# Kernel tuning notes

Measured on AMD Instinct MI355X. Metric: run time of the kernel, lower is better.

## Reference

```python
import jax, jax.numpy as jnp
import numpy as np

N = 100000   # nodes
E = 1600000  # edges (avg degree 16)
IN = 128     # in_channels
H = 64       # num_hidden -> conv1 out = 2*H = 128
RRELU_SLOPE = (1.0 / 8.0 + 1.0 / 3.0) / 2.0  # F.rrelu eval: mean of (lower, upper)


def setup_inputs() -> dict:
    key = jax.random.key(0)
    k1, k2, k3, k4 = jax.random.split(key, 4)
    x = jax.random.normal(k1, (N, IN), dtype=jnp.float32)
    edge_index = jax.random.randint(k2, (2, E), 0, N, dtype=jnp.int32)
    # Glorot-ish init for the two GCN linear layers (PyG GCNConv has weight + bias)
    W1 = jax.random.normal(k3, (IN, 2 * H), dtype=jnp.float32) * (1.0 / np.sqrt(IN))
    b1 = jnp.zeros((2 * H,), dtype=jnp.float32)
    W2 = jax.random.normal(k4, (2 * H, H), dtype=jnp.float32) * (1.0 / np.sqrt(2 * H))
    b2 = jnp.zeros((H,), dtype=jnp.float32)
    return {"x": x, "edge_index": edge_index, "W1": W1, "b1": b1, "W2": W2, "b2": b2}


def _gcn_conv(x, row, col, norm, W, b, n):
    # PyG GCNConv: transform, gather source nodes, scale by sym norm, scatter-add to targets
    h = x @ W                                   # [N, out]
    msg = h[row] * norm[:, None]                # [E+N, out] gathered messages
    return jax.ops.segment_sum(msg, col, num_segments=n) + b


def reference(x, edge_index, W1, b1, W2, b2):
    n = x.shape[0]
    loops = jnp.arange(n, dtype=edge_index.dtype)
    row = jnp.concatenate([edge_index[0], loops])  # sources (with self-loops)
    col = jnp.concatenate([edge_index[1], loops])  # targets (with self-loops)
    deg = jax.ops.segment_sum(jnp.ones_like(col, dtype=x.dtype), col, num_segments=n)
    dinv = jnp.where(deg > 0, jax.lax.rsqrt(deg), 0.0)
    norm = dinv[row] * dinv[col]                  # deg^{-1/2}[u] * deg^{-1/2}[v]
    h = _gcn_conv(x, row, col, norm, W1, b1, n)
    h = jnp.where(h >= 0, h, RRELU_SLOPE * h)     # rrelu (eval mode)
    return _gcn_conv(h, row, col, norm, W2, b2, n)
```

## Files before the change

### kernel.cpp

```cpp
#include <hip/hip_runtime.h>


#define C_IN   128
#define C_MID  128
#define C_OUT2 64
#define SLOT_CAP 64
#define SORT_SH  9
#define SORT_W   196
#define SORT_CAP 16384
#define P1_EPT   8

typedef __attribute__((ext_vector_type(8))) short short8;
typedef __attribute__((ext_vector_type(4))) float floatx4;
typedef __attribute__((ext_vector_type(2))) float f32x2;

__device__ __constant__ float kSlope = 0.22916666666666666f;

__device__ __forceinline__ unsigned short f2bf(float f) {
    unsigned u = __builtin_bit_cast(unsigned, f);
    u = (u + 0x7fffu + ((u >> 16) & 1u)) >> 16;
    return (unsigned short)u;
}
__device__ __forceinline__ f32x2 bfpair(int x) {
    return (f32x2){__builtin_bit_cast(float, (unsigned)x << 16),
                   __builtin_bit_cast(float, (unsigned)(x & 0xffff0000))};
}

__global__ __launch_bounds__(256) void sort_prep_kernel(
        const int* __restrict__ ei, int2* __restrict__ sorted,
        int* __restrict__ bcur,
        const float* __restrict__ W1, const float* __restrict__ W2,
        ushort* __restrict__ W1T, ushort* __restrict__ W2T,
        int E, int p1b) {
    if (blockIdx.x >= p1b) {
        int t = (blockIdx.x - p1b) * 256 + threadIdx.x;
        if (t < C_MID * C_IN) {
            int nn = t >> 7, k = t & 127;
            W1T[t] = f2bf(W1[k * C_MID + nn]);
        } else {
            int i = t - C_MID * C_IN;
            if (i < C_OUT2 * C_MID) {
                int nn = i >> 7, k = i & 127;
                W2T[i] = f2bf(W2[k * C_OUT2 + nn]);
            }
        }
        return;
    }
    __shared__ int hist[SORT_W], goff[SORT_W], cur[SORT_W];
    const int tid = threadIdx.x;
    for (int i = tid; i < SORT_W; i += 256) { hist[i] = 0; cur[i] = 0; }
    __syncthreads();
    const int base = blockIdx.x * (P1_EPT * 256);
#pragma unroll
    for (int k = 0; k < P1_EPT; ++k) {
        int e = base + k * 256 + tid;
        if (e < E) atomicAdd(&hist[ei[E + e] >> SORT_SH], 1);
    }
    __syncthreads();
    for (int i = tid; i < SORT_W; i += 256)
        if (hist[i]) goff[i] = atomicAdd(&bcur[i], hist[i]);
    __syncthreads();
#pragma unroll
    for (int k = 0; k < P1_EPT; ++k) {
        int e = base + k * 256 + tid;
        if (e < E) {
            int v = ei[E + e], u = ei[e];
            int b = v >> SORT_SH;
            int p = goff[b] + atomicAdd(&cur[b], 1);
            if (p < SORT_CAP) sorted[(size_t)b * SORT_CAP + p] = (int2){u, v};
        }
    }
}

template <int CO, bool ABF>
__device__ __forceinline__ void gemm_body(char* smem, int row0,
        const void* __restrict__ Xv, const ushort* __restrict__ WT,
        ushort* __restrict__ Y, int n) {
    constexpr int LDW = 136;
    constexpr int NT = CO / 16;
    ushort* Ws = (ushort*)smem;
    const int tid = threadIdx.x, wave = tid >> 6, lane = tid & 63;
    const int m = lane & 15, q = lane >> 4;

#pragma unroll
    for (int c = 0; c < CO / 16; ++c) {
        int id = tid + c * 256;
        int r = id >> 4, h8 = id & 15;
        *(int4*)&Ws[r * LDW + h8 * 8] = ((const int4*)(WT + r * C_IN))[h8];
    }
    __syncthreads();

    const int rowA = min(row0 + wave * 16 + m, n - 1);
    floatx4 acc[NT];
#pragma unroll
    for (int c = 0; c < NT; ++c) acc[c] = (floatx4){0.f, 0.f, 0.f, 0.f};

#pragma unroll
    for (int s = 0; s < 4; ++s) {
        short8 af;
        if constexpr (ABF) {
            af = *(const short8*)((const ushort*)Xv + (size_t)rowA * C_IN + s * 32 + q * 8);
        } else {
            const float* xp = (const float*)Xv + (size_t)rowA * C_IN + s * 32 + q * 8;
            float4 a0 = *(const float4*)xp;
            float4 a1 = *(const float4*)(xp + 4);
            union { unsigned short us[8]; short8 v; } t;
            t.us[0] = f2bf(a0.x); t.us[1] = f2bf(a0.y); t.us[2] = f2bf(a0.z); t.us[3] = f2bf(a0.w);
            t.us[4] = f2bf(a1.x); t.us[5] = f2bf(a1.y); t.us[6] = f2bf(a1.z); t.us[7] = f2bf(a1.w);
            af = t.v;
        }
#pragma unroll
        for (int c = 0; c < NT; ++c) {
            short8 bf = *(short8*)&Ws[(c * 16 + m) * LDW + s * 32 + q * 8];
            acc[c] = __builtin_amdgcn_mfma_f32_16x16x32_bf16(af, bf, acc[c], 0, 0, 0);
        }
    }
#pragma unroll
    for (int c = 0; c < NT; ++c)
#pragma unroll
        for (int i = 0; i < 4; ++i) {
            int rr = row0 + wave * 16 + q * 4 + i;
            if (rr < n) Y[(size_t)rr * CO + c * 16 + m] = f2bf(acc[c][i]);
        }
}

__global__ __launch_bounds__(256) void csr_gemm1_kernel(
        const int2* __restrict__ sorted, const int* __restrict__ bcur,
        int* __restrict__ cnt, float* __restrict__ dinv,
        int* __restrict__ slots,
        const float* __restrict__ X, const ushort* __restrict__ W1T,
        ushort* __restrict__ h1, int n) {
    __shared__ __align__(16) char smem[C_MID * 136 * 2];
    if (blockIdx.x < SORT_W) {
        int* lc = (int*)smem;
        const int b = blockIdx.x, tid = threadIdx.x;
        const int base_v = b << SORT_SH;
        for (int i = tid; i < 512; i += 256) lc[i] = 0;
        __syncthreads();
        const int nb = min(bcur[b], SORT_CAP);
        const int2* src = sorted + (size_t)b * SORT_CAP;
        for (int i = tid; i < nb; i += 256) {
            int2 e = src[i];
            int pos = atomicAdd(&lc[e.y - base_v], 1);
            if (pos < SLOT_CAP - 1) slots[(size_t)e.y * SLOT_CAP + pos] = e.x;
        }
        __syncthreads();
        for (int i = tid; i < 512; i += 256) {
            int v = base_v + i;
            if (v < n) {
                int deg = lc[i];
                int st = min(deg, SLOT_CAP - 1);
                slots[(size_t)v * SLOT_CAP + st] = v;
                cnt[v] = st + 1;
                dinv[v] = rsqrtf((float)(deg + 1));
            }
        }
        return;
    }
    gemm_body<C_MID, false>(smem, (blockIdx.x - SORT_W) * 64, X, W1T, h1, n);
}

template <int C, bool DO_RRELU, int OUT_MODE>
__global__ __launch_bounds__(256) void agg_kernel(const ushort* __restrict__ H,
                                                  const int* __restrict__ slots,
                                                  const int* __restrict__ cnt,
                                                  const float* __restrict__ dinv,
                                                  const float* __restrict__ bias,
                                                  void* __restrict__ outv, int n,
                                                  const ushort* __restrict__ W2T) {
    constexpr int GS = C / 8;
    constexpr int NG = 64 / GS;
    constexpr int NCH = 24 / NG;
    __shared__ ushort Hs[OUT_MODE == 2 ? 8 * 136 : 8];
    __shared__ int    Vs[8];
    const int wave = threadIdx.x >> 6, lane = threadIdx.x & 63;
    int vA = blockIdx.x * 8 + wave * 2;
    if constexpr (OUT_MODE == 2) {
        vA = min(vA, n - 2);
    } else {
        if (vA >= n) return;
    }
    const int vB = (vA + 1 < n) ? vA + 1 : vA;

    int rawA = slots[(size_t)vA * SLOT_CAP + lane];
    int rawB = slots[(size_t)vB * SLOT_CAP + lane];
    const int limA = cnt[vA], limB = cnt[vB];
    const float dvA = dinv[vA], dvB = dinv[vB];
    const int uA = min(max(rawA, 0), n - 1);
    const int uB = min(max(rawB, 0), n - 1);
    const float wA_l = dinv[uA] * dvA;
    const float wB_l = dinv[uB] * dvB;
    const int lastA = limA - 1, lastB = limB - 1;

    const int g = lane / GS, s = lane % GS;

    float wwA[NCH], wwB[NCH];
    int4 ddA[NCH], ddB[NCH];
#pragma unroll
    for (int t = 0; t < NCH; ++t) {
        int jj = t * NG + g;
        int cA = jj < lastA ? jj : lastA;
        int cB = jj < lastB ? jj : lastB;
        int usA = __shfl(uA, cA), usB = __shfl(uB, cB);
        float wsA = __shfl(wA_l, cA), wsB = __shfl(wB_l, cB);
        wwA[t] = (jj < limA) ? wsA : 0.f;
        wwB[t] = (jj < limB) ? wsB : 0.f;
        ddA[t] = *(const int4*)(H + (size_t)usA * C + s * 8);
        ddB[t] = *(const int4*)(H + (size_t)usB * C + s * 8);
    }
    __builtin_amdgcn_sched_barrier(0);

    f32x2 accA[4], accB[4];
#pragma unroll
    for (int k = 0; k < 4; ++k) { accA[k] = (f32x2){0.f, 0.f}; accB[k] = (f32x2){0.f, 0.f}; }
#pragma unroll
    for (int t = 0; t < NCH; ++t) {
        accA[0] += bfpair(ddA[t].x) * wwA[t]; accA[1] += bfpair(ddA[t].y) * wwA[t];
        accA[2] += bfpair(ddA[t].z) * wwA[t]; accA[3] += bfpair(ddA[t].w) * wwA[t];
        accB[0] += bfpair(ddB[t].x) * wwB[t]; accB[1] += bfpair(ddB[t].y) * wwB[t];
        accB[2] += bfpair(ddB[t].z) * wwB[t]; accB[3] += bfpair(ddB[t].w) * wwB[t];
    }
    for (int j = 24; j < limA; j += NG) {
        int jj = j + g;
        int c = jj < lastA ? jj : lastA;
        int u = __shfl(uA, c);
        float wv = __shfl(wA_l, c);
        float wgt = (jj < limA) ? wv : 0.f;
        const int4 d = *(const int4*)(H + (size_t)u * C + s * 8);
        accA[0] += bfpair(d.x) * wgt; accA[1] += bfpair(d.y) * wgt;
        accA[2] += bfpair(d.z) * wgt; accA[3] += bfpair(d.w) * wgt;
    }
    for (int j = 24; j < limB; j += NG) {
        int jj = j + g;
        int c = jj < lastB ? jj : lastB;
        int u = __shfl(uB, c);
        float wv = __shfl(wB_l, c);
        float wgt = (jj < limB) ? wv : 0.f;
        const int4 d = *(const int4*)(H + (size_t)u * C + s * 8);
        accB[0] += bfpair(d.x) * wgt; accB[1] += bfpair(d.y) * wgt;
        accB[2] += bfpair(d.z) * wgt; accB[3] += bfpair(d.w) * wgt;
    }

    float a[8], b8[8];
#pragma unroll
    for (int k = 0; k < 4; ++k) {
        a[2 * k] = accA[k].x; a[2 * k + 1] = accA[k].y;
        b8[2 * k] = accB[k].x; b8[2 * k + 1] = accB[k].y;
    }
#pragma unroll
    for (int k = 0; k < 8; ++k)
#pragma unroll
        for (int off = GS; off < 64; off <<= 1) {
            a[k] += __shfl_xor(a[k], off);
            b8[k] += __shfl_xor(b8[k], off);
        }

    if constexpr (OUT_MODE == 2) {
        if (g < 2) {
            const int v = (g == 0) ? vA : vB;
            union { ushort us[8]; int4 v4; } o;
#pragma unroll
            for (int k = 0; k < 8; ++k) {
                float t = (g == 0) ? a[k] : b8[k];
                t += bias[s * 8 + k];
                if (DO_RRELU) t = (t >= 0.f) ? t : t * kSlope;
                o.us[k] = f2bf(t);
            }
            *(int4*)&Hs[(wave * 2 + g) * 136 + s * 8] = o.v4;
            if (s == 0) Vs[wave * 2 + g] = v;
        }
        __syncthreads();
        const int m2 = lane & 15, q2 = lane >> 4;
        floatx4 acc2 = (floatx4){0.f, 0.f, 0.f, 0.f};
#pragma unroll
        for (int s2 = 0; s2 < 4; ++s2) {
            short8 af = *(short8*)&Hs[m2 * 136 + s2 * 32 + q2 * 8];
            short8 bf = *(const short8*)(W2T + (size_t)(wave * 16 + m2) * C_MID + s2 * 32 + q2 * 8);
            acc2 = __builtin_amdgcn_mfma_f32_16x16x32_bf16(af, bf, acc2, 0, 0, 0);
        }
        ushort* Y2 = (ushort*)outv;
#pragma unroll
        for (int i = 0; i < 4; ++i) {
            int node = q2 * 4 + i;
            if (node < 8)
                Y2[(size_t)Vs[node] * C_OUT2 + wave * 16 + m2] = f2bf(acc2[i]);
        }
    } else if (g < 2) {
        const int v = (g == 0) ? vA : vB;
        float r[8];
#pragma unroll
        for (int k = 0; k < 8; ++k) {
            float t = (g == 0) ? a[k] : b8[k];
            r[k] = t + bias[s * 8 + k];
            if (DO_RRELU) r[k] = (r[k] >= 0.f) ? r[k] : r[k] * kSlope;
        }
        float* op = (float*)outv + (size_t)v * C + s * 8;
        *(float4*)op       = (float4){r[0], r[1], r[2], r[3]};
        *(float4*)(op + 4) = (float4){r[4], r[5], r[6], r[7]};
    }
}

extern "C" void kernel_launch(void* const* d_in, const int* in_sizes, int n_in,
                              void* d_out, int out_size, void* d_ws, size_t ws_size,
                              hipStream_t stream) {
    const float* x  = (const float*)d_in[0];
    const int*   ei = (const int*)d_in[1];
    const float* W1 = (const float*)d_in[2];
    const float* b1 = (const float*)d_in[3];
    const float* W2 = (const float*)d_in[4];
    const float* b2 = (const float*)d_in[5];
    const int n = in_sizes[0] / C_IN;
    const int E = in_sizes[1] / 2;

    char* w = (char*)d_ws;
    auto alloc = [&](size_t bytes) -> char* {
        char* p = w; w += (bytes + 255) & ~(size_t)255; return p;
    };
    int*    cnt    = (int*)alloc((size_t)n * 4);
    float*  dinv   = (float*)alloc((size_t)n * 4);
    int*    slots  = (int*)alloc((size_t)n * SLOT_CAP * 4);
    ushort* h1     = (ushort*)alloc((size_t)n * C_MID * 2);
    ushort* h3     = (ushort*)alloc((size_t)n * C_OUT2 * 2);
    ushort* W1T    = (ushort*)alloc((size_t)C_MID * C_IN * 2);
    ushort* W2T    = (ushort*)alloc((size_t)C_OUT2 * C_MID * 2);
    int2*   sorted = (int2*)alloc((size_t)SORT_W * SORT_CAP * 8);
    int*    bcur   = (int*)alloc((size_t)SORT_W * 4);

    const int p1b = (E + P1_EPT * 256 - 1) / (P1_EPT * 256);
    const int prep_blocks = (C_MID * C_IN + C_OUT2 * C_MID + 255) / 256;
    const int gemm1_blocks = (n + 63) / 64;

    hipMemsetAsync(bcur, 0, (size_t)SORT_W * 4, stream);
    sort_prep_kernel<<<p1b + prep_blocks, 256, 0, stream>>>(
        ei, sorted, bcur, W1, W2, W1T, W2T, E, p1b);
    csr_gemm1_kernel<<<SORT_W + gemm1_blocks, 256, 0, stream>>>(
        sorted, bcur, cnt, dinv, slots, x, W1T, h1, n);
    agg_kernel<C_MID, true, 2><<<(n + 7) / 8, 256, 0, stream>>>(
        h1, slots, cnt, dinv, b1, h3, n, W2T);
    agg_kernel<C_OUT2, false, 0><<<(n + 7) / 8, 256, 0, stream>>>(
        h3, slots, cnt, dinv, b2, d_out, n, nullptr);
}
```

Measured before the change: 266.1 us.

## Fuse layer-2 GEMM per wave via shuffles, removing LDS staging and block barrier

The fused second-layer projection no longer stages aggregated rows in shared memory behind a block-wide barrier. Each wave packs its two aggregated nodes into bf16 pairs, redistributes them with lane shuffles into MFMA B-fragments, and computes all 64 output channels itself (W2 as the A operand) in four MFMA tiles. This removes the __syncthreads and LDS traffic and lets waves retire independently. In exchange each wave does four times the MFMA work, mostly on padding columns, and reads all of W2T rather than a 16-row slice.

```diff
diff --git a/kernel.cpp b/kernel.cpp
--- a/kernel.cpp
+++ b/kernel.cpp
@@ -171,15 +171,9 @@
     constexpr int GS = C / 8;
     constexpr int NG = 64 / GS;
     constexpr int NCH = 24 / NG;
-    __shared__ ushort Hs[OUT_MODE == 2 ? 8 * 136 : 8];
-    __shared__ int    Vs[8];
     const int wave = threadIdx.x >> 6, lane = threadIdx.x & 63;
-    int vA = blockIdx.x * 8 + wave * 2;
-    if constexpr (OUT_MODE == 2) {
-        vA = min(vA, n - 2);
-    } else {
-        if (vA >= n) return;
-    }
+    const int vA = blockIdx.x * 8 + wave * 2;
+    if (vA >= n) return;
     const int vB = (vA + 1 < n) ? vA + 1 : vA;
 
     int rawA = slots[(size_t)vA * SLOT_CAP + lane];
@@ -256,34 +250,50 @@
         }
 
     if constexpr (OUT_MODE == 2) {
-        if (g < 2) {
-            const int v = (g == 0) ? vA : vB;
-            union { ushort us[8]; int4 v4; } o;
-#pragma unroll
-            for (int k = 0; k < 8; ++k) {
-                float t = (g == 0) ? a[k] : b8[k];
-                t += bias[s * 8 + k];
-                if (DO_RRELU) t = (t >= 0.f) ? t : t * kSlope;
-                o.us[k] = f2bf(t);
-            }
-            *(int4*)&Hs[(wave * 2 + g) * 136 + s * 8] = o.v4;
-            if (s == 0) Vs[wave * 2 + g] = v;
-        }
-        __syncthreads();
-        const int m2 = lane & 15, q2 = lane >> 4;
-        floatx4 acc2 = (floatx4){0.f, 0.f, 0.f, 0.f};
+        const int nn = lane & 15;
+        const int q2 = lane >> 4;
+        int qsel[4];
+#pragma unroll
+        for (int i = 0; i < 4; ++i) {
+            float tA0 = a[2 * i]     + bias[nn * 8 + 2 * i];
+            float tA1 = a[2 * i + 1] + bias[nn * 8 + 2 * i + 1];
+            float tB0 = b8[2 * i]     + bias[nn * 8 + 2 * i];
+            float tB1 = b8[2 * i + 1] + bias[nn * 8 + 2 * i + 1];
+            if (DO_RRELU) {
+                tA0 = (tA0 >= 0.f) ? tA0 : tA0 * kSlope;
+                tA1 = (tA1 >= 0.f) ? tA1 : tA1 * kSlope;
+                tB0 = (tB0 >= 0.f) ? tB0 : tB0 * kSlope;
+                tB1 = (tB1 >= 0.f) ? tB1 : tB1 * kSlope;
+            }
+            int pA = (int)f2bf(tA0) | ((int)f2bf(tA1) << 16);
+            int pB = (int)f2bf(tB0) | ((int)f2bf(tB1) << 16);
+            qsel[i] = (q2 & 1) ? pB : pA;
+        }
+        short8 bfrag[4];
 #pragma unroll
         for (int s2 = 0; s2 < 4; ++s2) {
-            short8 af = *(short8*)&Hs[m2 * 136 + s2 * 32 + q2 * 8];
-            short8 bf = *(const short8*)(W2T + (size_t)(wave * 16 + m2) * C_MID + s2 * 32 + q2 * 8);
-            acc2 = __builtin_amdgcn_mfma_f32_16x16x32_bf16(af, bf, acc2, 0, 0, 0);
+            union { int w[4]; short8 v; } u;
+#pragma unroll
+            for (int i = 0; i < 4; ++i)
+                u.w[i] = __shfl(qsel[i], nn * 16 + s2 * 4 + q2);
+            bfrag[s2] = u.v;
         }
         ushort* Y2 = (ushort*)outv;
-#pragma unroll
-        for (int i = 0; i < 4; ++i) {
-            int node = q2 * 4 + i;
-            if (node < 8)
-                Y2[(size_t)Vs[node] * C_OUT2 + wave * 16 + m2] = f2bf(acc2[i]);
+        const int vSel = (nn == 0) ? vA : vB;
+#pragma unroll
+        for (int ct = 0; ct < 4; ++ct) {
+            floatx4 acc2 = (floatx4){0.f, 0.f, 0.f, 0.f};
+#pragma unroll
+            for (int s2 = 0; s2 < 4; ++s2) {
+                short8 af = *(const short8*)(W2T +
+                        (size_t)(ct * 16 + nn) * C_MID + s2 * 32 + q2 * 8);
+                acc2 = __builtin_amdgcn_mfma_f32_16x16x32_bf16(af, bfrag[s2], acc2, 0, 0, 0);
+            }
+            if (nn < 2) {
+#pragma unroll
+                for (int i = 0; i < 4; ++i)
+                    Y2[(size_t)vSel * C_OUT2 + ct * 16 + q2 * 4 + i] = f2bf(acc2[i]);
+            }
         }
     } else if (g < 2) {
         const int v = (g == 0) ? vA : vB;
```

Measured after the change: 312.6 us. 1.17x slower.

## Move GEMM1 into the sort kernel and split CSR build into its own launch

Applied to the files above, without the earlier changes.

Moves the first-layer GEMM out of the CSR-build kernel and into the edge-bucketing kernel, which now also handles the W2 conversion. Each GEMM block converts its W1 half-tiles to bf16 in shared memory itself, so the separate W1T pre-transpose is gone. The CSR slot building becomes a standalone kernel. The aim is to overlap the GEMM with the bucketing pass, which is dominated by atomics and scattered stores, and to drop the W1T dependency. The cost is that every GEMM block does a strided fp32 W1 read and conversion, plus an extra sync round.

```diff
diff --git a/kernel.cpp b/kernel.cpp
--- a/kernel.cpp
+++ b/kernel.cpp
@@ -26,138 +26,125 @@
                    __builtin_bit_cast(float, (unsigned)(x & 0xffff0000))};
 }
 
-__global__ __launch_bounds__(256) void sort_prep_kernel(
+__global__ __launch_bounds__(256) void sort_gemm1_kernel(
         const int* __restrict__ ei, int2* __restrict__ sorted,
         int* __restrict__ bcur,
+        const float* __restrict__ X,
         const float* __restrict__ W1, const float* __restrict__ W2,
-        ushort* __restrict__ W1T, ushort* __restrict__ W2T,
-        int E, int p1b) {
-    if (blockIdx.x >= p1b) {
-        int t = (blockIdx.x - p1b) * 256 + threadIdx.x;
-        if (t < C_MID * C_IN) {
+        ushort* __restrict__ W2T, ushort* __restrict__ h1,
+        int E, int n, int p1b, int g1b) {
+    __shared__ __align__(16) ushort Ws[64 * 136];
+    const int tid = threadIdx.x;
+
+    if (blockIdx.x < p1b) {
+        int* hist = (int*)Ws;
+        int* goff = hist + SORT_W;
+        int* cur  = goff + SORT_W;
+        for (int i = tid; i < SORT_W; i += 256) { hist[i] = 0; cur[i] = 0; }
+        __syncthreads();
+        const int base = blockIdx.x * (P1_EPT * 256);
+#pragma unroll
+        for (int k = 0; k < P1_EPT; ++k) {
+            int e = base + k * 256 + tid;
+            if (e < E) atomicAdd(&hist[ei[E + e] >> SORT_SH], 1);
+        }
+        __syncthreads();
+        for (int i = tid; i < SORT_W; i += 256)
+            if (hist[i]) goff[i] = atomicAdd(&bcur[i], hist[i]);
+        __syncthreads();
+#pragma unroll
+        for (int k = 0; k < P1_EPT; ++k) {
+            int e = base + k * 256 + tid;
+            if (e < E) {
+                int v = ei[E + e], u = ei[e];
+                int b = v >> SORT_SH;
+                int p = goff[b] + atomicAdd(&cur[b], 1);
+                if (p < SORT_CAP) sorted[(size_t)b * SORT_CAP + p] = (int2){u, v};
+            }
+        }
+        return;
+    }
+    if (blockIdx.x >= p1b + g1b) {
+        int t = (blockIdx.x - p1b - g1b) * 256 + tid;
+        if (t < C_OUT2 * C_MID) {
             int nn = t >> 7, k = t & 127;
-            W1T[t] = f2bf(W1[k * C_MID + nn]);
-        } else {
-            int i = t - C_MID * C_IN;
-            if (i < C_OUT2 * C_MID) {
-                int nn = i >> 7, k = i & 127;
-                W2T[i] = f2bf(W2[k * C_OUT2 + nn]);
+            W2T[t] = f2bf(W2[k * C_OUT2 + nn]);
+        }
+        return;
+    }
+    const int wave = tid >> 6, lane = tid & 63;
+    const int m = lane & 15, q = lane >> 4;
+    const int row0 = (blockIdx.x - p1b) * 64;
+    const int rowA = min(row0 + wave * 16 + m, n - 1);
+
+    short8 af[4];
+#pragma unroll
+    for (int s = 0; s < 4; ++s) {
+        const float* xp = X + (size_t)rowA * C_IN + s * 32 + q * 8;
+        float4 a0 = *(const float4*)xp;
+        float4 a1 = *(const float4*)(xp + 4);
+        union { unsigned short us[8]; short8 v; } t;
+        t.us[0] = f2bf(a0.x); t.us[1] = f2bf(a0.y); t.us[2] = f2bf(a0.z); t.us[3] = f2bf(a0.w);
+        t.us[4] = f2bf(a1.x); t.us[5] = f2bf(a1.y); t.us[6] = f2bf(a1.z); t.us[7] = f2bf(a1.w);
+        af[s] = t.v;
+    }
+    floatx4 acc[8];
+#pragma unroll
+    for (int c = 0; c < 8; ++c) acc[c] = (floatx4){0.f, 0.f, 0.f, 0.f};
+
+#pragma unroll
+    for (int h = 0; h < 2; ++h) {
+        __syncthreads();
+        for (int i = 0; i < 32; ++i) {
+            int idx = i * 256 + tid;
+            int k = idx >> 6, rl = idx & 63;
+            Ws[rl * 136 + k] = f2bf(W1[k * C_MID + h * 64 + rl]);
+        }
+        __syncthreads();
+#pragma unroll
+        for (int s = 0; s < 4; ++s)
+#pragma unroll
+            for (int c = 0; c < 4; ++c) {
+                short8 bf = *(short8*)&Ws[(c * 16 + m) * 136 + s * 32 + q * 8];
+                acc[h * 4 + c] = __builtin_amdgcn_mfma_f32_16x16x32_bf16(af[s], bf, acc[h * 4 + c], 0, 0, 0);
             }
-        }
-        return;
-    }
-    __shared__ int hist[SORT_W], goff[SORT_W], cur[SORT_W];
-    const int tid = threadIdx.x;
-    for (int i = tid; i < SORT_W; i += 256) { hist[i] = 0; cur[i] = 0; }
-    __syncthreads();
-    const int base = blockIdx.x * (P1_EPT * 256);
-#pragma unroll
-    for (int k = 0; k < P1_EPT; ++k) {
-        int e = base + k * 256 + tid;
-        if (e < E) atomicAdd(&hist[ei[E + e] >> SORT_SH], 1);
-    }
-    __syncthreads();
-    for (int i = tid; i < SORT_W; i += 256)
-        if (hist[i]) goff[i] = atomicAdd(&bcur[i], hist[i]);
-    __syncthreads();
-#pragma unroll
-    for (int k = 0; k < P1_EPT; ++k) {
-        int e = base + k * 256 + tid;
-        if (e < E) {
-            int v = ei[E + e], u = ei[e];
-            int b = v >> SORT_SH;
-            int p = goff[b] + atomicAdd(&cur[b], 1);
-            if (p < SORT_CAP) sorted[(size_t)b * SORT_CAP + p] = (int2){u, v};
-        }
-    }
-}
-
-template <int CO, bool ABF>
-__device__ __forceinline__ void gemm_body(char* smem, int row0,
-        const void* __restrict__ Xv, const ushort* __restrict__ WT,
-        ushort* __restrict__ Y, int n) {
-    constexpr int LDW = 136;
-    constexpr int NT = CO / 16;
-    ushort* Ws = (ushort*)smem;
-    const int tid = threadIdx.x, wave = tid >> 6, lane = tid & 63;
-    const int m = lane & 15, q = lane >> 4;
-
-#pragma unroll
-    for (int c = 0; c < CO / 16; ++c) {
-        int id = tid + c * 256;
-        int r = id >> 4, h8 = id & 15;
-        *(int4*)&Ws[r * LDW + h8 * 8] = ((const int4*)(WT + r * C_IN))[h8];
-    }
-    __syncthreads();
-
-    const int rowA = min(row0 + wave * 16 + m, n - 1);
-    floatx4 acc[NT];
-#pragma unroll
-    for (int c = 0; c < NT; ++c) acc[c] = (floatx4){0.f, 0.f, 0.f, 0.f};
-
-#pragma unroll
-    for (int s = 0; s < 4; ++s) {
-        short8 af;
-        if constexpr (ABF) {
-            af = *(const short8*)((const ushort*)Xv + (size_t)rowA * C_IN + s * 32 + q * 8);
-        } else {
-            const float* xp = (const float*)Xv + (size_t)rowA * C_IN + s * 32 + q * 8;
-            float4 a0 = *(const float4*)xp;
-            float4 a1 = *(const float4*)(xp + 4);
-            union { unsigned short us[8]; short8 v; } t;
-            t.us[0] = f2bf(a0.x); t.us[1] = f2bf(a0.y); t.us[2] = f2bf(a0.z); t.us[3] = f2bf(a0.w);
-            t.us[4] = f2bf(a1.x); t.us[5] = f2bf(a1.y); t.us[6] = f2bf(a1.z); t.us[7] = f2bf(a1.w);
-            af = t.v;
-        }
-#pragma unroll
-        for (int c = 0; c < NT; ++c) {
-            short8 bf = *(short8*)&Ws[(c * 16 + m) * LDW + s * 32 + q * 8];
-            acc[c] = __builtin_amdgcn_mfma_f32_16x16x32_bf16(af, bf, acc[c], 0, 0, 0);
-        }
-    }
-#pragma unroll
-    for (int c = 0; c < NT; ++c)
+    }
+#pragma unroll
+    for (int c = 0; c < 8; ++c)
 #pragma unroll
         for (int i = 0; i < 4; ++i) {
             int rr = row0 + wave * 16 + q * 4 + i;
-            if (rr < n) Y[(size_t)rr * CO + c * 16 + m] = f2bf(acc[c][i]);
-        }
-}
-
-__global__ __launch_bounds__(256) void csr_gemm1_kernel(
+            if (rr < n) h1[(size_t)rr * C_MID + c * 16 + m] = f2bf(acc[c][i]);
+        }
+}
+
+__global__ __launch_bounds__(256) void csr_kernel(
         const int2* __restrict__ sorted, const int* __restrict__ bcur,
         int* __restrict__ cnt, float* __restrict__ dinv,
-        int* __restrict__ slots,
-        const float* __restrict__ X, const ushort* __restrict__ W1T,
-        ushort* __restrict__ h1, int n) {
-    __shared__ __align__(16) char smem[C_MID * 136 * 2];
-    if (blockIdx.x < SORT_W) {
-        int* lc = (int*)smem;
-        const int b = blockIdx.x, tid = threadIdx.x;
-        const int base_v = b << SORT_SH;
-        for (int i = tid; i < 512; i += 256) lc[i] = 0;
-        __syncthreads();
-        const int nb = min(bcur[b], SORT_CAP);
-        const int2* src = sorted + (size_t)b * SORT_CAP;
-        for (int i = tid; i < nb; i += 256) {
-            int2 e = src[i];
-            int pos = atomicAdd(&lc[e.y - base_v], 1);
-            if (pos < SLOT_CAP - 1) slots[(size_t)e.y * SLOT_CAP + pos] = e.x;
-        }
-        __syncthreads();
-        for (int i = tid; i < 512; i += 256) {
-            int v = base_v + i;
-            if (v < n) {
-                int deg = lc[i];
-                int st = min(deg, SLOT_CAP - 1);
-                slots[(size_t)v * SLOT_CAP + st] = v;
-                cnt[v] = st + 1;
-                dinv[v] = rsqrtf((float)(deg + 1));
-            }
-        }
-        return;
-    }
-    gemm_body<C_MID, false>(smem, (blockIdx.x - SORT_W) * 64, X, W1T, h1, n);
+        int* __restrict__ slots, int n) {
+    __shared__ int lc[512];
+    const int b = blockIdx.x, tid = threadIdx.x;
+    const int base_v = b << SORT_SH;
+    for (int i = tid; i < 512; i += 256) lc[i] = 0;
+    __syncthreads();
+    const int nb = min(bcur[b], SORT_CAP);
+    const int2* src = sorted + (size_t)b * SORT_CAP;
+    for (int i = tid; i < nb; i += 256) {
+        int2 e = src[i];
+        int pos = atomicAdd(&lc[e.y - base_v], 1);
+        if (pos < SLOT_CAP - 1) slots[(size_t)e.y * SLOT_CAP + pos] = e.x;
+    }
+    __syncthreads();
+    for (int i = tid; i < 512; i += 256) {
+        int v = base_v + i;
+        if (v < n) {
+            int deg = lc[i];
+            int st = min(deg, SLOT_CAP - 1);
+            slots[(size_t)v * SLOT_CAP + st] = v;
+            cnt[v] = st + 1;
+            dinv[v] = rsqrtf((float)(deg + 1));
+        }
+    }
 }
 
 template <int C, bool DO_RRELU, int OUT_MODE>
@@ -321,20 +308,18 @@
     int*    slots  = (int*)alloc((size_t)n * SLOT_CAP * 4);
     ushort* h1     = (ushort*)alloc((size_t)n * C_MID * 2);
     ushort* h3     = (ushort*)alloc((size_t)n * C_OUT2 * 2);
-    ushort* W1T    = (ushort*)alloc((size_t)C_MID * C_IN * 2);
     ushort* W2T    = (ushort*)alloc((size_t)C_OUT2 * C_MID * 2);
     int2*   sorted = (int2*)alloc((size_t)SORT_W * SORT_CAP * 8);
     int*    bcur   = (int*)alloc((size_t)SORT_W * 4);
 
     const int p1b = (E + P1_EPT * 256 - 1) / (P1_EPT * 256);
-    const int prep_blocks = (C_MID * C_IN + C_OUT2 * C_MID + 255) / 256;
-    const int gemm1_blocks = (n + 63) / 64;
+    const int g1b = (n + 63) / 64;
+    const int prep2_blocks = (C_OUT2 * C_MID + 255) / 256;
 
     hipMemsetAsync(bcur, 0, (size_t)SORT_W * 4, stream);
-    sort_prep_kernel<<<p1b + prep_blocks, 256, 0, stream>>>(
-        ei, sorted, bcur, W1, W2, W1T, W2T, E, p1b);
-    csr_gemm1_kernel<<<SORT_W + gemm1_blocks, 256, 0, stream>>>(
-        sorted, bcur, cnt, dinv, slots, x, W1T, h1, n);
+    sort_gemm1_kernel<<<p1b + g1b + prep2_blocks, 256, 0, stream>>>(
+        ei, sorted, bcur, x, W1, W2, W2T, h1, E, n, p1b, g1b);
+    csr_kernel<<<SORT_W, 256, 0, stream>>>(sorted, bcur, cnt, dinv, slots, n);
     agg_kernel<C_MID, true, 2><<<(n + 7) / 8, 256, 0, stream>>>(
         h1, slots, cnt, dinv, b1, h3, n, W2T);
     agg_kernel<C_OUT2, false, 0><<<(n + 7) / 8, 256, 0, stream>>>(
```

New measurement: 270.3 us. No clear change (+1.6%).
